# Kernel optimization log

Hardware: AMD Instinct MI355X
Metric: run time of the kernel (lower is better)

Reference implementation:

```python
import jax, jax.numpy as jnp
import numpy as np
from jax import lax

# Stacked SimpleRNN (Keras): h_t = tanh(x_t @ W + h_{t-1} @ U + b).
# Dropout(0.5) is only active in training mode; this reference implements
# inference (training=None -> dropout disabled), matching model(x).

B, T, F = 512, 512, 78
HIDDENS = (16, 32, 64, 70)
NUM_CLASSES = 5


def _glorot(key, shape):
    fan_in, fan_out = shape[0], shape[1]
    lim = float(np.sqrt(6.0 / (fan_in + fan_out)))
    return jax.random.uniform(key, shape, jnp.float32, -lim, lim)


def setup_inputs() -> dict:
    key = jax.random.key(0)
    ks = jax.random.split(key, 16)
    x = jax.random.normal(ks[0], (B, T, F), jnp.float32)
    params = {}
    in_dim = F
    for i, h in enumerate(HIDDENS):
        params[f"W{i}"] = _glorot(ks[1 + 3 * i], (in_dim, h))
        params[f"U{i}"] = _glorot(ks[2 + 3 * i], (h, h))
        params[f"b{i}"] = jnp.zeros((h,), jnp.float32)
        in_dim = h
    params["Wd"] = _glorot(ks[13], (HIDDENS[-1], NUM_CLASSES))
    params["bd"] = jnp.zeros((NUM_CLASSES,), jnp.float32)
    return {"x": x, **params}


def _simple_rnn(x, W, U, b, return_sequences):
    # Precompute input projection for all timesteps: [B, T, H]
    xw = jnp.einsum("btf,fh->bth", x, W) + b
    h0 = jnp.zeros((x.shape[0], W.shape[1]), x.dtype)

    def step(h, xw_t):
        h_new = jnp.tanh(xw_t + h @ U)
        return h_new, h_new

    h_last, hs = lax.scan(step, h0, jnp.swapaxes(xw, 0, 1))  # scan over time
    if return_sequences:
        return jnp.swapaxes(hs, 0, 1)  # [B, T, H]
    return h_last  # [B, H]


def reference(x, W0, U0, b0, W1, U1, b1, W2, U2, b2, W3, U3, b3, Wd, bd):
    h = _simple_rnn(x, W0, U0, b0, True)
    h = _simple_rnn(h, W1, U1, b1, True)
    h = _simple_rnn(h, W2, U2, b2, True)
    h = _simple_rnn(h, W3, U3, b3, False)  # [B, 70]
    logits = h @ Wd + bd  # [B, 5]
    return jax.nn.softmax(logits, axis=-1)
```

## Files before the change

### kernel.cpp

```cpp
#include <hip/hip_runtime.h>
#include <cstddef>
#include <cstdint>


#define BB 512
#define TT 512
#define M_TOTAL (BB * TT)

__device__ __forceinline__ float tanh_fast(float x) {
  float ax = fabsf(x);
  float e = __expf(ax + ax);
  float r = 1.0f - 2.0f / (e + 1.0f);
  return (x >= 0.0f) ? r : -r;
}

__device__ __forceinline__ void fma4(float4& a, float s, const float4 w) {
  a.x = fmaf(s, w.x, a.x);
  a.y = fmaf(s, w.y, a.y);
  a.z = fmaf(s, w.z, a.z);
  a.w = fmaf(s, w.w, a.w);
}

template<int K, int N, int CG>
__global__ __launch_bounds__(256)
void proj_kernel(const float* __restrict__ in, const float* __restrict__ W,
                 const float* __restrict__ bias, float* __restrict__ out, int M)
{
  constexpr int NP = CG * 4;
  constexpr int RG = 256 / CG;
  __shared__ __align__(16) float wlds[K][NP];
  __shared__ __align__(16) float blds[NP];
  const int tid = threadIdx.x;
  for (int idx = tid; idx < K * NP; idx += 256) {
    int k = idx / NP, jj = idx - k * NP;
    wlds[k][jj] = (jj < N) ? W[k * N + jj] : 0.0f;
  }
  if (tid < NP) blds[tid] = (tid < N) ? bias[tid] : 0.0f;
  __syncthreads();

  const int c = tid % CG;
  const int rg = tid / CG;
  if (rg >= RG) return;
  const int j0 = c * 4;
  const long row0 = (long)blockIdx.x * (RG * 4) + (long)rg * 4;

  float4 b4 = *reinterpret_cast<const float4*>(&blds[j0]);
  float4 acc[4] = {b4, b4, b4, b4};
  const float* inp[4];
  bool rv[4];
  #pragma unroll
  for (int rr = 0; rr < 4; ++rr) {
    long rowi = row0 + rr;
    rv[rr] = rowi < M;
    inp[rr] = in + (rv[rr] ? rowi : 0) * (long)K;
  }

  int k = 0;
  for (; k + 4 <= K; k += 4) {
    float4 w0 = *reinterpret_cast<const float4*>(&wlds[k + 0][j0]);
    float4 w1 = *reinterpret_cast<const float4*>(&wlds[k + 1][j0]);
    float4 w2 = *reinterpret_cast<const float4*>(&wlds[k + 2][j0]);
    float4 w3 = *reinterpret_cast<const float4*>(&wlds[k + 3][j0]);
    #pragma unroll
    for (int rr = 0; rr < 4; ++rr) {
      float2 i0 = *reinterpret_cast<const float2*>(inp[rr] + k);
      float2 i1 = *reinterpret_cast<const float2*>(inp[rr] + k + 2);
      fma4(acc[rr], i0.x, w0);
      fma4(acc[rr], i0.y, w1);
      fma4(acc[rr], i1.x, w2);
      fma4(acc[rr], i1.y, w3);
    }
  }
  for (; k < K; ++k) {
    float4 w0 = *reinterpret_cast<const float4*>(&wlds[k][j0]);
    #pragma unroll
    for (int rr = 0; rr < 4; ++rr) fma4(acc[rr], inp[rr][k], w0);
  }

  #pragma unroll
  for (int rr = 0; rr < 4; ++rr) {
    if (!rv[rr]) continue;
    long obase = (row0 + rr) * (long)N + j0;
    if constexpr ((N % 4) == 0) {
      *reinterpret_cast<float4*>(&out[obase]) = acc[rr];
    } else {
      if (j0 + 4 <= N) {
        *reinterpret_cast<float2*>(&out[obase]) = make_float2(acc[rr].x, acc[rr].y);
        *reinterpret_cast<float2*>(&out[obase + 2]) = make_float2(acc[rr].z, acc[rr].w);
      } else {
        float v[4] = {acc[rr].x, acc[rr].y, acc[rr].z, acc[rr].w};
        #pragma unroll
        for (int jj = 0; jj < 4; ++jj)
          if (j0 + jj < N) out[obase + jj] = v[jj];
      }
    }
  }
}

template<int H, int ROWS>
__global__ __launch_bounds__(64, 1)
void rec_kernel(const float* __restrict__ xw, const float* __restrict__ U,
                float* __restrict__ hseq)
{
  constexpr int HP = (H + 3) & ~3;
  constexpr int PF = 8;
  const int tid = threadIdx.x;
  const int r = tid / H;
  const int j = tid - r * H;
  const int row = blockIdx.x * ROWS + r;

  __shared__ __align__(16) float hlds[ROWS][HP];
  for (int i = tid; i < ROWS * HP; i += 64)
    reinterpret_cast<float*>(hlds)[i] = 0.0f;
  __syncthreads();

  float u[HP];
  #pragma unroll
  for (int kk = 0; kk < HP; ++kk) {
    u[kk] = (kk < H) ? U[kk * H + j] : 0.0f;
    asm volatile("" : "+v"(u[kk]));
  }

  const float* xwrow = xw + ((size_t)row * TT) * H + j;
  float* hout = hseq + ((size_t)row * TT) * H + j;

  float pf[PF];
  #pragma unroll
  for (int d = 0; d < PF; ++d) pf[d] = xwrow[(size_t)d * H];

  for (int t = 0; t < TT; t += PF) {
    #pragma unroll
    for (int d = 0; d < PF; ++d) {
      float xv = pf[d];
      int tn = t + d + PF;
      tn = (tn < TT) ? tn : (TT - 1);
      pf[d] = xwrow[(size_t)tn * H];

      const float* hb = &hlds[r][0];
      float a0 = xv, a1 = 0.0f, a2 = 0.0f, a3 = 0.0f;
      #pragma unroll
      for (int k4 = 0; k4 < HP / 4; ++k4) {
        float4 h4 = *reinterpret_cast<const float4*>(hb + 4 * k4);
        a0 = fmaf(h4.x, u[4 * k4 + 0], a0);
        a1 = fmaf(h4.y, u[4 * k4 + 1], a1);
        a2 = fmaf(h4.z, u[4 * k4 + 2], a2);
        a3 = fmaf(h4.w, u[4 * k4 + 3], a3);
      }
      float hn = tanh_fast((a0 + a1) + (a2 + a3));
      hlds[r][j] = hn;
      hout[(size_t)(t + d) * H] = hn;
    }
  }
}

__global__ __launch_bounds__(64, 1)
void rec70_kernel(const float* __restrict__ xw, const float* __restrict__ U,
                  const float* __restrict__ Wd, const float* __restrict__ bd,
                  float* __restrict__ outp)
{
  constexpr int H = 70, HP = 72, PF = 8;
  const int tid = threadIdx.x;
  const int row = blockIdx.x;
  const int j2 = (tid < 6) ? (64 + tid) : 69;

  __shared__ __align__(16) float hlds[HP];
  for (int i = tid; i < HP; i += 64) hlds[i] = 0.0f;
  __syncthreads();

  float u[HP], u2[HP];
  #pragma unroll
  for (int kk = 0; kk < HP; ++kk) {
    u[kk]  = (kk < H) ? U[kk * H + tid] : 0.0f;
    u2[kk] = (kk < H && tid < 6) ? U[kk * H + 64 + tid] : 0.0f;
    asm volatile("" : "+v"(u[kk]), "+v"(u2[kk]));
  }

  const float* xwrow = xw + ((size_t)row * TT) * H;
  float pfA[PF], pfB[PF];
  #pragma unroll
  for (int d = 0; d < PF; ++d) {
    pfA[d] = xwrow[(size_t)d * H + tid];
    pfB[d] = xwrow[(size_t)d * H + j2];
  }

  for (int t = 0; t < TT; t += PF) {
    #pragma unroll
    for (int d = 0; d < PF; ++d) {
      float xvA = pfA[d], xvB = pfB[d];
      int tn = t + d + PF;
      tn = (tn < TT) ? tn : (TT - 1);
      pfA[d] = xwrow[(size_t)tn * H + tid];
      pfB[d] = xwrow[(size_t)tn * H + j2];

      float a0 = xvA, a1 = 0.0f, a2 = 0.0f, a3 = 0.0f;
      float b0 = xvB, b1 = 0.0f, b2 = 0.0f, b3 = 0.0f;
      #pragma unroll
      for (int k4 = 0; k4 < HP / 4; ++k4) {
        float4 h4 = *reinterpret_cast<const float4*>(&hlds[4 * k4]);
        a0 = fmaf(h4.x, u[4 * k4 + 0], a0);
        a1 = fmaf(h4.y, u[4 * k4 + 1], a1);
        a2 = fmaf(h4.z, u[4 * k4 + 2], a2);
        a3 = fmaf(h4.w, u[4 * k4 + 3], a3);
        b0 = fmaf(h4.x, u2[4 * k4 + 0], b0);
        b1 = fmaf(h4.y, u2[4 * k4 + 1], b1);
        b2 = fmaf(h4.z, u2[4 * k4 + 2], b2);
        b3 = fmaf(h4.w, u2[4 * k4 + 3], b3);
      }
      float hnA = tanh_fast((a0 + a1) + (a2 + a3));
      float hnB = tanh_fast((b0 + b1) + (b2 + b3));
      hlds[tid] = hnA;
      if (tid < 6) hlds[64 + tid] = hnB;
    }
  }

  float l = 0.0f;
  if (tid < 5) {
    l = bd[tid];
    #pragma unroll
    for (int kk = 0; kk < H; ++kk)
      l = fmaf(hlds[kk], Wd[kk * 5 + tid], l);
  }
  float l0 = __shfl(l, 0), l1 = __shfl(l, 1), l2 = __shfl(l, 2),
        l3 = __shfl(l, 3), l4 = __shfl(l, 4);
  float m = fmaxf(fmaxf(fmaxf(l0, l1), fmaxf(l2, l3)), l4);
  float s = __expf(l0 - m) + __expf(l1 - m) + __expf(l2 - m) +
            __expf(l3 - m) + __expf(l4 - m);
  if (tid < 5)
    outp[(size_t)row * 5 + tid] = __expf(l - m) / s;
}

extern "C" void kernel_launch(void* const* d_in, const int* in_sizes, int n_in,
                              void* d_out, int out_size, void* d_ws, size_t ws_size,
                              hipStream_t stream)
{
  const float* x  = (const float*)d_in[0];
  const float* W0 = (const float*)d_in[1];
  const float* U0 = (const float*)d_in[2];
  const float* b0 = (const float*)d_in[3];
  const float* W1 = (const float*)d_in[4];
  const float* U1 = (const float*)d_in[5];
  const float* b1 = (const float*)d_in[6];
  const float* W2 = (const float*)d_in[7];
  const float* U2 = (const float*)d_in[8];
  const float* b2 = (const float*)d_in[9];
  const float* W3 = (const float*)d_in[10];
  const float* U3 = (const float*)d_in[11];
  const float* b3 = (const float*)d_in[12];
  const float* Wd = (const float*)d_in[13];
  const float* bd = (const float*)d_in[14];
  float* outp = (float*)d_out;

  float* A  = (float*)d_ws;
  float* Bv = (float*)((char*)d_ws + 73400320);

  const int M = M_TOTAL;

  proj_kernel<78, 16, 4><<<M / 256, 256, 0, stream>>>(x, W0, b0, A, M);
  rec_kernel<16, 4><<<BB / 4, 64, 0, stream>>>(A, U0, Bv);
  proj_kernel<16, 32, 8><<<M / 128, 256, 0, stream>>>(Bv, W1, b1, A, M);
  rec_kernel<32, 2><<<BB / 2, 64, 0, stream>>>(A, U1, Bv);
  proj_kernel<32, 64, 16><<<M / 64, 256, 0, stream>>>(Bv, W2, b2, A, M);
  rec_kernel<64, 1><<<BB, 64, 0, stream>>>(A, U2, Bv);
  proj_kernel<64, 70, 18><<<(M + 55) / 56, 256, 0, stream>>>(Bv, W3, b3, A, M);
  rec70_kernel<<<BB, 64, 0, stream>>>(A, U3, Wd, bd, outp);
}
```

Before: 962.2 us.

## Fuse next-layer input projections into recurrent kernels and split rec70 across two waves

```diff
diff --git a/kernel.cpp b/kernel.cpp
--- a/kernel.cpp
+++ b/kernel.cpp
@@ -6,6 +6,8 @@
 #define BB 512
 #define TT 512
 #define M_TOTAL (BB * TT)
+
+#define LDS_BARRIER() asm volatile("s_waitcnt lgkmcnt(0)\n\ts_barrier" ::: "memory")
 
 __device__ __forceinline__ float tanh_fast(float x) {
   float ax = fabsf(x);
@@ -97,32 +99,31 @@
   }
 }
 
-template<int H, int ROWS>
 __global__ __launch_bounds__(64, 1)
-void rec_kernel(const float* __restrict__ xw, const float* __restrict__ U,
-                float* __restrict__ hseq)
-{
-  constexpr int HP = (H + 3) & ~3;
-  constexpr int PF = 8;
-  const int tid = threadIdx.x;
-  const int r = tid / H;
-  const int j = tid - r * H;
-  const int row = blockIdx.x * ROWS + r;
-
-  __shared__ __align__(16) float hlds[ROWS][HP];
-  for (int i = tid; i < ROWS * HP; i += 64)
-    reinterpret_cast<float*>(hlds)[i] = 0.0f;
-  __syncthreads();
-
-  float u[HP];
-  #pragma unroll
-  for (int kk = 0; kk < HP; ++kk) {
-    u[kk] = (kk < H) ? U[kk * H + j] : 0.0f;
-    asm volatile("" : "+v"(u[kk]));
-  }
-
-  const float* xwrow = xw + ((size_t)row * TT) * H + j;
-  float* hout = hseq + ((size_t)row * TT) * H + j;
+void fused_rec16(const float* __restrict__ xw, const float* __restrict__ U,
+                 const float* __restrict__ Wn, const float* __restrict__ bn,
+                 float* __restrict__ xwn)
+{
+  constexpr int H = 16, ROWS = 4, HN = 32, PF = 8;
+  const int tid = threadIdx.x;
+  const int r = tid >> 4, j = tid & 15;
+  const int c = tid & 31, pr = tid >> 5;
+  __shared__ __align__(16) float hlds[ROWS][H];
+  for (int i = tid; i < ROWS * H; i += 64) reinterpret_cast<float*>(hlds)[i] = 0.0f;
+  __syncthreads();
+
+  float u[H], w[H];
+  #pragma unroll
+  for (int kk = 0; kk < H; ++kk) {
+    u[kk] = U[kk * H + j];
+    w[kk] = Wn[kk * HN + c];
+    asm volatile("" : "+v"(u[kk]), "+v"(w[kk]));
+  }
+  const float bc = bn[c];
+
+  const float* xwrow = xw + ((size_t)(blockIdx.x * ROWS + r) * TT) * H + j;
+  float* o0 = xwn + ((size_t)(blockIdx.x * ROWS + 2 * pr + 0) * TT) * HN + c;
+  float* o1 = xwn + ((size_t)(blockIdx.x * ROWS + 2 * pr + 1) * TT) * HN + c;
 
   float pf[PF];
   #pragma unroll
@@ -137,6 +138,199 @@
       pf[d] = xwrow[(size_t)tn * H];
 
       const float* hb = &hlds[r][0];
+      float a0 = xv, a1 = 0.0f, a2 = 0.0f, a3 = 0.0f;
+      #pragma unroll
+      for (int k4 = 0; k4 < H / 4; ++k4) {
+        float4 h4 = *reinterpret_cast<const float4*>(hb + 4 * k4);
+        a0 = fmaf(h4.x, u[4 * k4 + 0], a0);
+        a1 = fmaf(h4.y, u[4 * k4 + 1], a1);
+        a2 = fmaf(h4.z, u[4 * k4 + 2], a2);
+        a3 = fmaf(h4.w, u[4 * k4 + 3], a3);
+      }
+      float hn = tanh_fast((a0 + a1) + (a2 + a3));
+      hlds[r][j] = hn;
+
+      const float* h0b = &hlds[2 * pr + 0][0];
+      const float* h1b = &hlds[2 * pr + 1][0];
+      float s0 = bc, s1 = bc, s2 = 0.0f, s3 = 0.0f;
+      #pragma unroll
+      for (int k4 = 0; k4 < H / 4; ++k4) {
+        float4 ha = *reinterpret_cast<const float4*>(h0b + 4 * k4);
+        float4 hc = *reinterpret_cast<const float4*>(h1b + 4 * k4);
+        s0 = fmaf(ha.x, w[4 * k4 + 0], s0);
+        s2 = fmaf(ha.y, w[4 * k4 + 1], s2);
+        s0 = fmaf(ha.z, w[4 * k4 + 2], s0);
+        s2 = fmaf(ha.w, w[4 * k4 + 3], s2);
+        s1 = fmaf(hc.x, w[4 * k4 + 0], s1);
+        s3 = fmaf(hc.y, w[4 * k4 + 1], s3);
+        s1 = fmaf(hc.z, w[4 * k4 + 2], s1);
+        s3 = fmaf(hc.w, w[4 * k4 + 3], s3);
+      }
+      o0[(size_t)(t + d) * HN] = s0 + s2;
+      o1[(size_t)(t + d) * HN] = s1 + s3;
+    }
+  }
+}
+
+__global__ __launch_bounds__(64, 1)
+void fused_rec32(const float* __restrict__ xw, const float* __restrict__ U,
+                 const float* __restrict__ Wn, const float* __restrict__ bn,
+                 float* __restrict__ xwn)
+{
+  constexpr int H = 32, ROWS = 2, HN = 64, PF = 8;
+  const int tid = threadIdx.x;
+  const int r = tid >> 5, j = tid & 31;
+  const int c = tid;
+  __shared__ __align__(16) float hlds[ROWS][H];
+  for (int i = tid; i < ROWS * H; i += 64) reinterpret_cast<float*>(hlds)[i] = 0.0f;
+  __syncthreads();
+
+  float u[H], w[H];
+  #pragma unroll
+  for (int kk = 0; kk < H; ++kk) {
+    u[kk] = U[kk * H + j];
+    w[kk] = Wn[kk * HN + c];
+    asm volatile("" : "+v"(u[kk]), "+v"(w[kk]));
+  }
+  const float bc = bn[c];
+
+  const float* xwrow = xw + ((size_t)(blockIdx.x * ROWS + r) * TT) * H + j;
+  float* o0 = xwn + ((size_t)(blockIdx.x * ROWS + 0) * TT) * HN + c;
+  float* o1 = xwn + ((size_t)(blockIdx.x * ROWS + 1) * TT) * HN + c;
+
+  float pf[PF];
+  #pragma unroll
+  for (int d = 0; d < PF; ++d) pf[d] = xwrow[(size_t)d * H];
+
+  for (int t = 0; t < TT; t += PF) {
+    #pragma unroll
+    for (int d = 0; d < PF; ++d) {
+      float xv = pf[d];
+      int tn = t + d + PF;
+      tn = (tn < TT) ? tn : (TT - 1);
+      pf[d] = xwrow[(size_t)tn * H];
+
+      const float* hb = &hlds[r][0];
+      float a0 = xv, a1 = 0.0f, a2 = 0.0f, a3 = 0.0f;
+      #pragma unroll
+      for (int k4 = 0; k4 < H / 4; ++k4) {
+        float4 h4 = *reinterpret_cast<const float4*>(hb + 4 * k4);
+        a0 = fmaf(h4.x, u[4 * k4 + 0], a0);
+        a1 = fmaf(h4.y, u[4 * k4 + 1], a1);
+        a2 = fmaf(h4.z, u[4 * k4 + 2], a2);
+        a3 = fmaf(h4.w, u[4 * k4 + 3], a3);
+      }
+      float hn = tanh_fast((a0 + a1) + (a2 + a3));
+      hlds[r][j] = hn;
+
+      const float* h0b = &hlds[0][0];
+      const float* h1b = &hlds[1][0];
+      float s0 = bc, s1 = bc, s2 = 0.0f, s3 = 0.0f;
+      #pragma unroll
+      for (int k4 = 0; k4 < H / 4; ++k4) {
+        float4 ha = *reinterpret_cast<const float4*>(h0b + 4 * k4);
+        float4 hc = *reinterpret_cast<const float4*>(h1b + 4 * k4);
+        s0 = fmaf(ha.x, w[4 * k4 + 0], s0);
+        s2 = fmaf(ha.y, w[4 * k4 + 1], s2);
+        s0 = fmaf(ha.z, w[4 * k4 + 2], s0);
+        s2 = fmaf(ha.w, w[4 * k4 + 3], s2);
+        s1 = fmaf(hc.x, w[4 * k4 + 0], s1);
+        s3 = fmaf(hc.y, w[4 * k4 + 1], s3);
+        s1 = fmaf(hc.z, w[4 * k4 + 2], s1);
+        s3 = fmaf(hc.w, w[4 * k4 + 3], s3);
+      }
+      o0[(size_t)(t + d) * HN] = s0 + s2;
+      o1[(size_t)(t + d) * HN] = s1 + s3;
+    }
+  }
+}
+
+__global__ __launch_bounds__(64, 1)
+void rec64_kernel(const float* __restrict__ xw, const float* __restrict__ U,
+                  float* __restrict__ hseq)
+{
+  constexpr int H = 64, PF = 8;
+  const int tid = threadIdx.x;
+  const int row = blockIdx.x;
+
+  __shared__ __align__(16) float hlds[H];
+  hlds[tid] = 0.0f;
+  __syncthreads();
+
+  float u[H];
+  #pragma unroll
+  for (int kk = 0; kk < H; ++kk) {
+    u[kk] = U[kk * H + tid];
+    asm volatile("" : "+v"(u[kk]));
+  }
+
+  const float* xwrow = xw + ((size_t)row * TT) * H + tid;
+  float* hout = hseq + ((size_t)row * TT) * H + tid;
+
+  float pf[PF];
+  #pragma unroll
+  for (int d = 0; d < PF; ++d) pf[d] = xwrow[(size_t)d * H];
+
+  for (int t = 0; t < TT; t += PF) {
+    #pragma unroll
+    for (int d = 0; d < PF; ++d) {
+      float xv = pf[d];
+      int tn = t + d + PF;
+      tn = (tn < TT) ? tn : (TT - 1);
+      pf[d] = xwrow[(size_t)tn * H];
+
+      float a0 = xv, a1 = 0.0f, a2 = 0.0f, a3 = 0.0f;
+      #pragma unroll
+      for (int k4 = 0; k4 < H / 4; ++k4) {
+        float4 h4 = *reinterpret_cast<const float4*>(&hlds[4 * k4]);
+        a0 = fmaf(h4.x, u[4 * k4 + 0], a0);
+        a1 = fmaf(h4.y, u[4 * k4 + 1], a1);
+        a2 = fmaf(h4.z, u[4 * k4 + 2], a2);
+        a3 = fmaf(h4.w, u[4 * k4 + 3], a3);
+      }
+      float hn = tanh_fast((a0 + a1) + (a2 + a3));
+      hlds[tid] = hn;
+      hout[(size_t)(t + d) * H] = hn;
+    }
+  }
+}
+
+__global__ __launch_bounds__(128, 1)
+void rec70_kernel(const float* __restrict__ xw, const float* __restrict__ U,
+                  const float* __restrict__ Wd, const float* __restrict__ bd,
+                  float* __restrict__ outp)
+{
+  constexpr int H = 70, HP = 72, PF = 8;
+  const int tid = threadIdx.x;
+  const int row = blockIdx.x;
+  const bool act = tid < H;
+  const int j = act ? tid : 0;
+
+  __shared__ __align__(16) float hbuf[2][HP];
+  for (int i = tid; i < 2 * HP; i += 128) reinterpret_cast<float*>(hbuf)[i] = 0.0f;
+  __syncthreads();
+
+  float u[HP];
+  #pragma unroll
+  for (int kk = 0; kk < HP; ++kk) {
+    u[kk] = (kk < H && act) ? U[kk * H + j] : 0.0f;
+    asm volatile("" : "+v"(u[kk]));
+  }
+
+  const float* xwrow = xw + ((size_t)row * TT) * H + j;
+  float pf[PF];
+  #pragma unroll
+  for (int d = 0; d < PF; ++d) pf[d] = xwrow[(size_t)d * H];
+
+  for (int t = 0; t < TT; t += PF) {
+    #pragma unroll
+    for (int d = 0; d < PF; ++d) {
+      float xv = pf[d];
+      int tn = t + d + PF;
+      tn = (tn < TT) ? tn : (TT - 1);
+      pf[d] = xwrow[(size_t)tn * H];
+
+      const float* hb = &hbuf[(t + d) & 1][0];
       float a0 = xv, a1 = 0.0f, a2 = 0.0f, a3 = 0.0f;
       #pragma unroll
       for (int k4 = 0; k4 < HP / 4; ++k4) {
@@ -147,69 +341,8 @@
         a3 = fmaf(h4.w, u[4 * k4 + 3], a3);
       }
       float hn = tanh_fast((a0 + a1) + (a2 + a3));
-      hlds[r][j] = hn;
-      hout[(size_t)(t + d) * H] = hn;
-    }
-  }
-}
-
-__global__ __launch_bounds__(64, 1)
-void rec70_kernel(const float* __restrict__ xw, const float* __restrict__ U,
-                  const float* __restrict__ Wd, const float* __restrict__ bd,
-                  float* __restrict__ outp)
-{
-  constexpr int H = 70, HP = 72, PF = 8;
-  const int tid = threadIdx.x;
-  const int row = blockIdx.x;
-  const int j2 = (tid < 6) ? (64 + tid) : 69;
-
-  __shared__ __align__(16) float hlds[HP];
-  for (int i = tid; i < HP; i += 64) hlds[i] = 0.0f;
-  __syncthreads();
-
-  float u[HP], u2[HP];
-  #pragma unroll
-  for (int kk = 0; kk < HP; ++kk) {
-    u[kk]  = (kk < H) ? U[kk * H + tid] : 0.0f;
-    u2[kk] = (kk < H && tid < 6) ? U[kk * H + 64 + tid] : 0.0f;
-    asm volatile("" : "+v"(u[kk]), "+v"(u2[kk]));
-  }
-
-  const float* xwrow = xw + ((size_t)row * TT) * H;
-  float pfA[PF], pfB[PF];
-  #pragma unroll
-  for (int d = 0; d < PF; ++d) {
-    pfA[d] = xwrow[(size_t)d * H + tid];
-    pfB[d] = xwrow[(size_t)d * H + j2];
-  }
-
-  for (int t = 0; t < TT; t += PF) {
-    #pragma unroll
-    for (int d = 0; d < PF; ++d) {
-      float xvA = pfA[d], xvB = pfB[d];
-      int tn = t + d + PF;
-      tn = (tn < TT) ? tn : (TT - 1);
-      pfA[d] = xwrow[(size_t)tn * H + tid];
-      pfB[d] = xwrow[(size_t)tn * H + j2];
-
-      float a0 = xvA, a1 = 0.0f, a2 = 0.0f, a3 = 0.0f;
-      float b0 = xvB, b1 = 0.0f, b2 = 0.0f, b3 = 0.0f;
-      #pragma unroll
-      for (int k4 = 0; k4 < HP / 4; ++k4) {
-        float4 h4 = *reinterpret_cast<const float4*>(&hlds[4 * k4]);
-        a0 = fmaf(h4.x, u[4 * k4 + 0], a0);
-        a1 = fmaf(h4.y, u[4 * k4 + 1], a1);
-        a2 = fmaf(h4.z, u[4 * k4 + 2], a2);
-        a3 = fmaf(h4.w, u[4 * k4 + 3], a3);
-        b0 = fmaf(h4.x, u2[4 * k4 + 0], b0);
-        b1 = fmaf(h4.y, u2[4 * k4 + 1], b1);
-        b2 = fmaf(h4.z, u2[4 * k4 + 2], b2);
-        b3 = fmaf(h4.w, u2[4 * k4 + 3], b3);
-      }
-      float hnA = tanh_fast((a0 + a1) + (a2 + a3));
-      float hnB = tanh_fast((b0 + b1) + (b2 + b3));
-      hlds[tid] = hnA;
-      if (tid < 6) hlds[64 + tid] = hnB;
+      if (act) hbuf[((t + d) & 1) ^ 1][j] = hn;
+      LDS_BARRIER();
     }
   }
 
@@ -218,7 +351,7 @@
     l = bd[tid];
     #pragma unroll
     for (int kk = 0; kk < H; ++kk)
-      l = fmaf(hlds[kk], Wd[kk * 5 + tid], l);
+      l = fmaf(hbuf[0][kk], Wd[kk * 5 + tid], l);
   }
   float l0 = __shfl(l, 0), l1 = __shfl(l, 1), l2 = __shfl(l, 2),
         l3 = __shfl(l, 3), l4 = __shfl(l, 4);
@@ -256,11 +389,9 @@
   const int M = M_TOTAL;
 
   proj_kernel<78, 16, 4><<<M / 256, 256, 0, stream>>>(x, W0, b0, A, M);
-  rec_kernel<16, 4><<<BB / 4, 64, 0, stream>>>(A, U0, Bv);
-  proj_kernel<16, 32, 8><<<M / 128, 256, 0, stream>>>(Bv, W1, b1, A, M);
-  rec_kernel<32, 2><<<BB / 2, 64, 0, stream>>>(A, U1, Bv);
-  proj_kernel<32, 64, 16><<<M / 64, 256, 0, stream>>>(Bv, W2, b2, A, M);
-  rec_kernel<64, 1><<<BB, 64, 0, stream>>>(A, U2, Bv);
+  fused_rec16<<<BB / 4, 64, 0, stream>>>(A, U0, W1, b1, Bv);
+  fused_rec32<<<BB / 2, 64, 0, stream>>>(Bv, U1, W2, b2, A);
+  rec64_kernel<<<BB, 64, 0, stream>>>(A, U2, Bv);
   proj_kernel<64, 70, 18><<<(M + 55) / 56, 256, 0, stream>>>(Bv, W3, b3, A, M);
-  rec70_kernel<<<BB, 64, 0, stream>>>(A, U3, Wd, bd, outp);
-}
+  rec70_kernel<<<BB, 128, 0, stream>>>(A, U3, Wd, bd, outp);
+}
```

Measured after the change: 1.152 ms. 19.7% more time.
